# Kernel optimization log

Measured on AMD Instinct MI355X. Metric: run time of the kernel, lower is better.

Reference implementation:

```python
import jax, jax.numpy as jnp
import numpy as np

N, CIN, COUT, H, W, K = 2, 64, 64, 256, 512, 3


def _gen_sphere_position(height, width, Kh, Kw):
    # Faithful numpy port of SphereConv.gen_sphere_position (ERP type).
    delta_lat = np.pi / height
    delta_lon = 2 * np.pi / width
    range_x = np.arange(-(Kw // 2), Kw // 2 + 1)
    if not Kw % 2:
        range_x = np.delete(range_x, Kw // 2)
    range_y = np.arange(-(Kh // 2), Kh // 2 + 1)
    if not Kh % 2:
        range_y = np.delete(range_y, Kh // 2)
    kerX = np.tan(range_x * delta_lon)
    kerY = np.tan(range_y * delta_lat) / np.cos(range_y * delta_lon)
    kerX, kerY = np.meshgrid(kerX, kerY)
    rho = np.sqrt(kerX ** 2 + kerY ** 2)
    if Kh % 2 and Kw % 2:
        rho[Kh // 2][Kw // 2] = 1e-08
    nu = np.arctan(rho)
    cos_nu, sin_nu = np.cos(nu), np.sin(nu)
    lat_range = (np.arange(height) / height - 0.5) * np.pi
    lon_range = (np.arange(width) / width - 0.5) * (2 * np.pi)
    lat = np.array([np.arcsin(cos_nu * np.sin(l) + kerY * sin_nu * np.cos(l) / rho) for l in lat_range])  # (H,Kh,Kw)
    lat = np.array([lat for _ in lon_range]).transpose((1, 0, 2, 3))  # (H,W,Kh,Kw)
    lon = np.array([np.arctan2(kerX * sin_nu, rho * np.cos(l) * cos_nu - kerY * np.sin(l) * sin_nu) for l in lat_range])  # (H,Kh,Kw)
    lon = np.array([lon + _lon for _lon in lon_range]).transpose((1, 0, 2, 3))  # (H,W,Kh,Kw)
    lat = (lat / np.pi + 0.5) * height
    lon = (lon / (2 * np.pi) + 0.5) * width % width
    LatLon = np.stack((lat, lon)).astype(np.float32)  # (2,H,W,Kh,Kw)
    LatLon = LatLon.transpose((3, 4, 0, 1, 2)).reshape(Kh * Kw * 2, height, width)  # channel = (i*Kw+j)*2 + {0:lat,1:lon}
    return LatLon


def setup_inputs() -> dict:
    key = jax.random.key(0)
    kx, kw = jax.random.split(key)
    x = jax.random.normal(kx, (N, CIN, H, W), dtype=jnp.float32)
    n = CIN * K * K
    stdv = 1.0 / np.sqrt(n)
    weight = jax.random.uniform(kw, (COUT, CIN, K, K), dtype=jnp.float32, minval=-stdv, maxval=stdv)
    position = jnp.asarray(_gen_sphere_position(H, W, K, K))  # (2*K*K, H, W)
    return {"x": x, "weight": weight, "position": position}


def _sphere_conv(x, weight, position):
    # x: [N,C,H,W]; position: [2*K2,Hout,Wout] absolute (lat=y, lon=x) sample coords per kernel tap.
    Cout, Cin, Kh, Kw = weight.shape
    K2 = Kh * Kw
    Hi, Wi = x.shape[2], x.shape[3]
    pos = position.reshape(K2, 2, position.shape[-2], position.shape[-1])
    py, px = pos[:, 0], pos[:, 1]  # [K2,Hout,Wout]
    y0 = jnp.floor(py)
    x0 = jnp.floor(px)
    dy = py - y0
    dx = px - x0

    def corner(yi, xi, wgt):
        valid = (yi >= 0) & (yi <= Hi - 1) & (xi >= 0) & (xi <= Wi - 1)
        yc = jnp.clip(yi, 0, Hi - 1).astype(jnp.int32)
        xc = jnp.clip(xi, 0, Wi - 1).astype(jnp.int32)
        v = x[:, :, yc, xc]  # gather -> [N,C,K2,Hout,Wout]
        return v * (wgt * valid)[None, None]

    sampled = (corner(y0, x0, (1 - dy) * (1 - dx))
               + corner(y0, x0 + 1, (1 - dy) * dx)
               + corner(y0 + 1, x0, dy * (1 - dx))
               + corner(y0 + 1, x0 + 1, dy * dx))  # [N,C,K2,Hout,Wout]
    w = weight.reshape(Cout, Cin, K2)
    return jnp.einsum('ock,nckhw->nohw', w, sampled)


def reference(x, weight, position):
    return _sphere_conv(x, weight, position)
```

## Files before the change

kernel.cpp:

```cpp
#include <hip/hip_runtime.h>
#include <hip/hip_bf16.h>


constexpr int N_ = 2;
constexpr int CIN = 64;
constexpr int COUT = 64;
constexpr int H_ = 256;
constexpr int W_ = 512;
constexpr int K2 = 9;
constexpr int HW = H_ * W_;
constexpr int NSTEP = (CIN * K2) / 32;
constexpr int PTILE = 128;
constexpr int SROW = 40;

typedef __attribute__((ext_vector_type(8))) short short8;
typedef __attribute__((ext_vector_type(4))) float floatx4;
typedef __attribute__((ext_vector_type(2))) float floatx2;

__device__ __forceinline__ float bfhi2f(unsigned u) {
  return __uint_as_float(u);
}

__global__ void prep_w(const float* __restrict__ w, ushort* __restrict__ wTr) {
  int i = blockIdx.x * blockDim.x + threadIdx.x;
  if (i >= 4 * NSTEP * 64 * 8) return;
  int j = i & 7;
  int lane = (i >> 3) & 63;
  int s = (i >> 9) % NSTEP;
  int wv = i / (512 * NSTEP);
  int o = wv * 16 + (lane & 15);
  int kk = s * 32 + (lane >> 4) * 8 + j;
  int tap = kk >> 6, c = kk & 63;
  __hip_bfloat16 b = __float2bfloat16(w[(o * CIN + c) * K2 + tap]);
  wTr[i] = *(ushort*)&b;
}

__global__ __launch_bounds__(256) void transpose_x(
    const float* __restrict__ x, ushort* __restrict__ xt) {
  __shared__ ushort tile[64 * 72];
  int b = blockIdx.x;
  int n = b >> 11;
  int hw0 = (b & 2047) * 64;
  int tid = threadIdx.x;
  int px = tid & 63, c4 = tid >> 6;
  const float* xn = x + (size_t)n * CIN * HW;
#pragma unroll
  for (int it = 0; it < 16; ++it) {
    int c = it * 4 + c4;
    float v = xn[(size_t)c * HW + hw0 + px];
    __hip_bfloat16 hb = __float2bfloat16(v);
    tile[px * 72 + c] = *(ushort*)&hb;
  }
  __syncthreads();
  ushort* xtn = xt + (size_t)n * HW * CIN;
#pragma unroll
  for (int it = 0; it < 2; ++it) {
    int task = it * 256 + tid;
    int px2 = task >> 3, chunk = task & 7;
    uint4 v = *(uint4*)&tile[px2 * 72 + chunk * 8];
    *(uint4*)&xtn[(size_t)(hw0 + px2) * 64 + chunk * 8] = v;
  }
}

__global__ __launch_bounds__(256, 3) void sphere_conv_mfma(
    const ushort* __restrict__ xt, const ushort* __restrict__ wTr,
    const float* __restrict__ pos, float* __restrict__ out) {
  __shared__ int off_lds[K2 * PTILE];
  __shared__ uint2 wgt_lds[K2 * PTILE];
  __shared__ ushort sbuf[2][PTILE * SROW];

  int tid = threadIdx.x;
  int blk = blockIdx.x;
  int n = blk >> 10;
  int ptile = (blk & 1023) * PTILE;

  for (int i = tid; i < K2 * PTILE; i += 256) {
    int t = i / PTILE, p = i - t * PTILE;
    int hw = ptile + p;
    float py = pos[(2 * t + 0) * HW + hw];
    float px = pos[(2 * t + 1) * HW + hw];
    float y0f = floorf(py), x0f = floorf(px);
    float dy = py - y0f, dx = px - x0f;
    float y1f = y0f + 1.f, x1f = x0f + 1.f;
    float vy0 = (y0f >= 0.f && y0f <= (float)(H_ - 1)) ? 1.f : 0.f;
    float vy1 = (y1f >= 0.f && y1f <= (float)(H_ - 1)) ? 1.f : 0.f;
    float vx0 = (x0f >= 0.f && x0f <= (float)(W_ - 1)) ? 1.f : 0.f;
    float vx1 = (x1f >= 0.f && x1f <= (float)(W_ - 1)) ? 1.f : 0.f;
    float w00 = (1.f - dy) * (1.f - dx) * vy0 * vx0;
    float w01 = (1.f - dy) * dx * vy0 * vx1;
    float w10 = dy * (1.f - dx) * vy1 * vx0;
    float w11 = dy * dx * vy1 * vx1;
    int y0c = (int)fminf(fmaxf(y0f, 0.f), (float)(H_ - 1));
    int y1c = (int)fminf(fmaxf(y1f, 0.f), (float)(H_ - 1));
    int x0c = (int)fminf(fmaxf(x0f, 0.f), (float)(W_ - 1));
    int x1c = (int)fminf(fmaxf(x1f, 0.f), (float)(W_ - 1));
    int o00 = y0c * W_ + x0c;
    off_lds[i] = o00 | ((x1c - x0c) << 20) | ((y1c - y0c) << 21);
    __hip_bfloat16 b00 = __float2bfloat16(w00), b01 = __float2bfloat16(w01);
    __hip_bfloat16 b10 = __float2bfloat16(w10), b11 = __float2bfloat16(w11);
    unsigned lo = ((unsigned)*(ushort*)&b01 << 16) | *(ushort*)&b00;
    unsigned hi = ((unsigned)*(ushort*)&b11 << 16) | *(ushort*)&b10;
    wgt_lds[i] = make_uint2(lo, hi);
  }

  int lane = tid & 63, wv = tid >> 6;
  int col = lane & 15, quad = lane >> 4;
  int px_s = tid >> 1, hf = tid & 1;

  floatx4 acc[8];
#pragma unroll
  for (int nt = 0; nt < 8; ++nt) acc[nt] = (floatx4)0.f;

  const ushort* xtn = xt + (size_t)n * HW * CIN;

  __syncthreads();

  auto gather = [&](int s, short8 g[8], float w4[4]) {
    int t = s >> 1;
    int c0 = ((s & 1) << 5) + (hf << 4);
    int pk = off_lds[t * PTILE + px_s];
    uint2 wr = wgt_lds[t * PTILE + px_s];
    w4[0] = bfhi2f(wr.x << 16);
    w4[1] = bfhi2f(wr.x & 0xFFFF0000u);
    w4[2] = bfhi2f(wr.y << 16);
    w4[3] = bfhi2f(wr.y & 0xFFFF0000u);
    int o00 = pk & 0x1FFFF;
    int dx1 = (pk >> 20) & 1;
    int dyW = ((pk >> 21) & 1) * W_;
    const ushort* base = xtn + c0;
    const ushort* p00 = base + (size_t)o00 * 64;
    const ushort* p01 = p00 + dx1 * 64;
    const ushort* p10 = p00 + dyW * 64;
    const ushort* p11 = p10 + dx1 * 64;
    g[0] = *(const short8*)p00; g[1] = *(const short8*)(p00 + 8);
    g[2] = *(const short8*)p01; g[3] = *(const short8*)(p01 + 8);
    g[4] = *(const short8*)p10; g[5] = *(const short8*)(p10 + 8);
    g[6] = *(const short8*)p11; g[7] = *(const short8*)(p11 + 8);
  };

  short8 gA[8];
  float wA[4];
  gather(0, gA, wA);

#pragma unroll
  for (int s = 0; s < NSTEP; ++s) {
    short8 gB[8];
    float wB[4];
    if (s + 1 < NSTEP) gather(s + 1, gB, wB);

    const unsigned* u = (const unsigned*)gA;
    floatx2 a2[8];
#pragma unroll
    for (int d = 0; d < 8; ++d) {
      floatx2 f = {bfhi2f(u[d] << 16), bfhi2f(u[d] & 0xFFFF0000u)};
      a2[d] = floatx2{wA[0], wA[0]} * f;
    }
#pragma unroll
    for (int c = 1; c < 4; ++c) {
#pragma unroll
      for (int d = 0; d < 8; ++d) {
        unsigned v = u[c * 8 + d];
        floatx2 f = {bfhi2f(v << 16), bfhi2f(v & 0xFFFF0000u)};
        a2[d] = __builtin_elementwise_fma(floatx2{wA[c], wA[c]}, f, a2[d]);
      }
    }
    __align__(16) unsigned tmp[8];
#pragma unroll
    for (int d = 0; d < 8; ++d) {
      __hip_bfloat16 lo = __float2bfloat16(a2[d].x);
      __hip_bfloat16 hi = __float2bfloat16(a2[d].y);
      tmp[d] = ((unsigned)*(ushort*)&hi << 16) | *(ushort*)&lo;
    }
    uint4* dst = (uint4*)&sbuf[s & 1][px_s * SROW + hf * 16];
    dst[0] = ((const uint4*)tmp)[0];
    dst[1] = ((const uint4*)tmp)[1];

    __syncthreads();

    short8 afrag = *(const short8*)(wTr + ((wv * NSTEP + s) * 64 + lane) * 8);
#pragma unroll
    for (int nt = 0; nt < 8; ++nt) {
      short8 bfrag = *(const short8*)&sbuf[s & 1][(nt * 16 + col) * SROW + quad * 8];
      acc[nt] = __builtin_amdgcn_mfma_f32_16x16x32_bf16(afrag, bfrag, acc[nt], 0, 0, 0);
    }

    if (s + 1 < NSTEP) {
#pragma unroll
      for (int q = 0; q < 8; ++q) gA[q] = gB[q];
#pragma unroll
      for (int q = 0; q < 4; ++q) wA[q] = wB[q];
    }
  }

#pragma unroll
  for (int nt = 0; nt < 8; ++nt) {
#pragma unroll
    for (int r = 0; r < 4; ++r) {
      int o = wv * 16 + quad * 4 + r;
      out[(size_t)(n * COUT + o) * HW + ptile + nt * 16 + col] = acc[nt][r];
    }
  }
}

extern "C" void kernel_launch(void* const* d_in, const int* in_sizes, int n_in,
                              void* d_out, int out_size, void* d_ws, size_t ws_size,
                              hipStream_t stream) {
  const float* x   = (const float*)d_in[0];
  const float* w   = (const float*)d_in[1];
  const float* pos = (const float*)d_in[2];
  float* out = (float*)d_out;

  ushort* wTr = (ushort*)d_ws;
  ushort* xt = (ushort*)((char*)d_ws + (128 << 10));

  prep_w<<<(4 * NSTEP * 64 * 8 + 255) / 256, 256, 0, stream>>>(w, wTr);
  transpose_x<<<N_ * (HW / 64), 256, 0, stream>>>(x, xt);

  int nblk = N_ * (HW / PTILE);
  sphere_conv_mfma<<<nblk, 256, 0, stream>>>(xt, wTr, pos, out);
}
```

Baseline: 208.8 us.

## Gather bilinear samples directly into MFMA B fragments, removing LDS staging

The main kernel now has each wave own 32 output pixels and all 64 output channels. Each lane gathers and interpolates its own 8-channel slice straight into the MFMA B-fragment layout, so the LDS offset/weight tables, the LDS sample buffer and the per-step block barriers are gone. Positions are decoded per lane in registers, and occupancy is raised to 4 blocks per SIMD. The transpose kernel also switches to float4 loads. In exchange, each lane reloads the weight A-fragments from global memory at every step, the position math is recomputed per lane, and the explicit prefetch of the next step's gathers is lost.

```diff
diff --git a/kernel.cpp b/kernel.cpp
--- a/kernel.cpp
+++ b/kernel.cpp
@@ -11,7 +11,6 @@
 constexpr int HW = H_ * W_;
 constexpr int NSTEP = (CIN * K2) / 32;
 constexpr int PTILE = 128;
-constexpr int SROW = 40;
 
 typedef __attribute__((ext_vector_type(8))) short short8;
 typedef __attribute__((ext_vector_type(4))) float floatx4;
@@ -27,8 +26,8 @@
   int j = i & 7;
   int lane = (i >> 3) & 63;
   int s = (i >> 9) % NSTEP;
-  int wv = i / (512 * NSTEP);
-  int o = wv * 16 + (lane & 15);
+  int ot = i / (512 * NSTEP);
+  int o = ot * 16 + (lane & 15);
   int kk = s * 32 + (lane >> 4) * 8 + j;
   int tap = kk >> 6, c = kk & 63;
   __hip_bfloat16 b = __float2bfloat16(w[(o * CIN + c) * K2 + tap]);
@@ -42,14 +41,21 @@
   int n = b >> 11;
   int hw0 = (b & 2047) * 64;
   int tid = threadIdx.x;
-  int px = tid & 63, c4 = tid >> 6;
+  int px4 = (tid & 15) * 4;
+  int cq = tid >> 4;
   const float* xn = x + (size_t)n * CIN * HW;
 #pragma unroll
-  for (int it = 0; it < 16; ++it) {
-    int c = it * 4 + c4;
-    float v = xn[(size_t)c * HW + hw0 + px];
-    __hip_bfloat16 hb = __float2bfloat16(v);
-    tile[px * 72 + c] = *(ushort*)&hb;
+  for (int it = 0; it < 4; ++it) {
+    int c = it * 16 + cq;
+    float4 v = *(const float4*)&xn[(size_t)c * HW + hw0 + px4];
+    __hip_bfloat16 b0 = __float2bfloat16(v.x);
+    __hip_bfloat16 b1 = __float2bfloat16(v.y);
+    __hip_bfloat16 b2 = __float2bfloat16(v.z);
+    __hip_bfloat16 b3 = __float2bfloat16(v.w);
+    tile[(px4 + 0) * 72 + c] = *(ushort*)&b0;
+    tile[(px4 + 1) * 72 + c] = *(ushort*)&b1;
+    tile[(px4 + 2) * 72 + c] = *(ushort*)&b2;
+    tile[(px4 + 3) * 72 + c] = *(ushort*)&b3;
   }
   __syncthreads();
   ushort* xtn = xt + (size_t)n * HW * CIN;
@@ -62,144 +68,123 @@
   }
 }
 
-__global__ __launch_bounds__(256, 3) void sphere_conv_mfma(
+__global__ __launch_bounds__(256, 4) void sphere_conv_mfma(
     const ushort* __restrict__ xt, const ushort* __restrict__ wTr,
     const float* __restrict__ pos, float* __restrict__ out) {
-  __shared__ int off_lds[K2 * PTILE];
-  __shared__ uint2 wgt_lds[K2 * PTILE];
-  __shared__ ushort sbuf[2][PTILE * SROW];
-
   int tid = threadIdx.x;
   int blk = blockIdx.x;
   int n = blk >> 10;
   int ptile = (blk & 1023) * PTILE;
-
-  for (int i = tid; i < K2 * PTILE; i += 256) {
-    int t = i / PTILE, p = i - t * PTILE;
-    int hw = ptile + p;
-    float py = pos[(2 * t + 0) * HW + hw];
-    float px = pos[(2 * t + 1) * HW + hw];
-    float y0f = floorf(py), x0f = floorf(px);
-    float dy = py - y0f, dx = px - x0f;
-    float y1f = y0f + 1.f, x1f = x0f + 1.f;
-    float vy0 = (y0f >= 0.f && y0f <= (float)(H_ - 1)) ? 1.f : 0.f;
-    float vy1 = (y1f >= 0.f && y1f <= (float)(H_ - 1)) ? 1.f : 0.f;
-    float vx0 = (x0f >= 0.f && x0f <= (float)(W_ - 1)) ? 1.f : 0.f;
-    float vx1 = (x1f >= 0.f && x1f <= (float)(W_ - 1)) ? 1.f : 0.f;
-    float w00 = (1.f - dy) * (1.f - dx) * vy0 * vx0;
-    float w01 = (1.f - dy) * dx * vy0 * vx1;
-    float w10 = dy * (1.f - dx) * vy1 * vx0;
-    float w11 = dy * dx * vy1 * vx1;
-    int y0c = (int)fminf(fmaxf(y0f, 0.f), (float)(H_ - 1));
-    int y1c = (int)fminf(fmaxf(y1f, 0.f), (float)(H_ - 1));
-    int x0c = (int)fminf(fmaxf(x0f, 0.f), (float)(W_ - 1));
-    int x1c = (int)fminf(fmaxf(x1f, 0.f), (float)(W_ - 1));
-    int o00 = y0c * W_ + x0c;
-    off_lds[i] = o00 | ((x1c - x0c) << 20) | ((y1c - y0c) << 21);
-    __hip_bfloat16 b00 = __float2bfloat16(w00), b01 = __float2bfloat16(w01);
-    __hip_bfloat16 b10 = __float2bfloat16(w10), b11 = __float2bfloat16(w11);
-    unsigned lo = ((unsigned)*(ushort*)&b01 << 16) | *(ushort*)&b00;
-    unsigned hi = ((unsigned)*(ushort*)&b11 << 16) | *(ushort*)&b10;
-    wgt_lds[i] = make_uint2(lo, hi);
-  }
-
   int lane = tid & 63, wv = tid >> 6;
   int col = lane & 15, quad = lane >> 4;
-  int px_s = tid >> 1, hf = tid & 1;
-
-  floatx4 acc[8];
-#pragma unroll
-  for (int nt = 0; nt < 8; ++nt) acc[nt] = (floatx4)0.f;
+
+  int hw[2];
+  hw[0] = ptile + wv * 32 + col;
+  hw[1] = hw[0] + 16;
 
   const ushort* xtn = xt + (size_t)n * HW * CIN;
 
-  __syncthreads();
-
-  auto gather = [&](int s, short8 g[8], float w4[4]) {
-    int t = s >> 1;
-    int c0 = ((s & 1) << 5) + (hf << 4);
-    int pk = off_lds[t * PTILE + px_s];
-    uint2 wr = wgt_lds[t * PTILE + px_s];
-    w4[0] = bfhi2f(wr.x << 16);
-    w4[1] = bfhi2f(wr.x & 0xFFFF0000u);
-    w4[2] = bfhi2f(wr.y << 16);
-    w4[3] = bfhi2f(wr.y & 0xFFFF0000u);
-    int o00 = pk & 0x1FFFF;
-    int dx1 = (pk >> 20) & 1;
-    int dyW = ((pk >> 21) & 1) * W_;
-    const ushort* base = xtn + c0;
-    const ushort* p00 = base + (size_t)o00 * 64;
-    const ushort* p01 = p00 + dx1 * 64;
-    const ushort* p10 = p00 + dyW * 64;
-    const ushort* p11 = p10 + dx1 * 64;
-    g[0] = *(const short8*)p00; g[1] = *(const short8*)(p00 + 8);
-    g[2] = *(const short8*)p01; g[3] = *(const short8*)(p01 + 8);
-    g[4] = *(const short8*)p10; g[5] = *(const short8*)(p10 + 8);
-    g[6] = *(const short8*)p11; g[7] = *(const short8*)(p11 + 8);
-  };
-
-  short8 gA[8];
-  float wA[4];
-  gather(0, gA, wA);
+  floatx4 acc[2][4];
+#pragma unroll
+  for (int T = 0; T < 2; ++T)
+#pragma unroll
+    for (int ot = 0; ot < 4; ++ot) acc[T][ot] = (floatx4)0.f;
+
+  int o00[2], dxo[2], dyo[2];
+  float w4[2][4];
 
 #pragma unroll
   for (int s = 0; s < NSTEP; ++s) {
-    short8 gB[8];
-    float wB[4];
-    if (s + 1 < NSTEP) gather(s + 1, gB, wB);
-
-    const unsigned* u = (const unsigned*)gA;
-    floatx2 a2[8];
-#pragma unroll
-    for (int d = 0; d < 8; ++d) {
-      floatx2 f = {bfhi2f(u[d] << 16), bfhi2f(u[d] & 0xFFFF0000u)};
-      a2[d] = floatx2{wA[0], wA[0]} * f;
+    if ((s & 1) == 0) {
+      int t = s >> 1;
+#pragma unroll
+      for (int T = 0; T < 2; ++T) {
+        float py = pos[(2 * t + 0) * HW + hw[T]];
+        float pxx = pos[(2 * t + 1) * HW + hw[T]];
+        float y0f = floorf(py), x0f = floorf(pxx);
+        float dy = py - y0f, dx = pxx - x0f;
+        float y1f = y0f + 1.f, x1f = x0f + 1.f;
+        float vy0 = (y0f >= 0.f && y0f <= (float)(H_ - 1)) ? 1.f : 0.f;
+        float vy1 = (y1f >= 0.f && y1f <= (float)(H_ - 1)) ? 1.f : 0.f;
+        float vx0 = (x0f >= 0.f && x0f <= (float)(W_ - 1)) ? 1.f : 0.f;
+        float vx1 = (x1f >= 0.f && x1f <= (float)(W_ - 1)) ? 1.f : 0.f;
+        w4[T][0] = (1.f - dy) * (1.f - dx) * vy0 * vx0;
+        w4[T][1] = (1.f - dy) * dx * vy0 * vx1;
+        w4[T][2] = dy * (1.f - dx) * vy1 * vx0;
+        w4[T][3] = dy * dx * vy1 * vx1;
+        int y0c = (int)fminf(fmaxf(y0f, 0.f), (float)(H_ - 1));
+        int y1c = (int)fminf(fmaxf(y1f, 0.f), (float)(H_ - 1));
+        int x0c = (int)fminf(fmaxf(x0f, 0.f), (float)(W_ - 1));
+        int x1c = (int)fminf(fmaxf(x1f, 0.f), (float)(W_ - 1));
+        o00[T] = (y0c * W_ + x0c) * CIN;
+        dxo[T] = (x1c - x0c) * CIN;
+        dyo[T] = (y1c - y0c) * (W_ * CIN);
+      }
     }
-#pragma unroll
-    for (int c = 1; c < 4; ++c) {
-#pragma unroll
-      for (int d = 0; d < 8; ++d) {
-        unsigned v = u[c * 8 + d];
-        floatx2 f = {bfhi2f(v << 16), bfhi2f(v & 0xFFFF0000u)};
-        a2[d] = __builtin_elementwise_fma(floatx2{wA[c], wA[c]}, f, a2[d]);
-      }
+    int c0 = ((s & 1) << 5) + (quad << 3);
+
+    short8 g[2][4];
+#pragma unroll
+    for (int T = 0; T < 2; ++T) {
+      const ushort* p00 = xtn + (size_t)o00[T] + c0;
+      const ushort* p10 = p00 + dyo[T];
+      g[T][0] = *(const short8*)p00;
+      g[T][1] = *(const short8*)(p00 + dxo[T]);
+      g[T][2] = *(const short8*)p10;
+      g[T][3] = *(const short8*)(p10 + dxo[T]);
     }
-    __align__(16) unsigned tmp[8];
-#pragma unroll
-    for (int d = 0; d < 8; ++d) {
-      __hip_bfloat16 lo = __float2bfloat16(a2[d].x);
-      __hip_bfloat16 hi = __float2bfloat16(a2[d].y);
-      tmp[d] = ((unsigned)*(ushort*)&hi << 16) | *(ushort*)&lo;
+
+    short8 afr[4];
+#pragma unroll
+    for (int ot = 0; ot < 4; ++ot)
+      afr[ot] = *(const short8*)(wTr + ((size_t)(ot * NSTEP + s) * 64 + lane) * 8);
+
+    short8 bfr[2];
+#pragma unroll
+    for (int T = 0; T < 2; ++T) {
+      const unsigned* u = (const unsigned*)&g[T][0];
+      floatx2 a2[4];
+#pragma unroll
+      for (int d = 0; d < 4; ++d) {
+        floatx2 f = {bfhi2f(u[d] << 16), bfhi2f(u[d] & 0xFFFF0000u)};
+        a2[d] = floatx2{w4[T][0], w4[T][0]} * f;
+      }
+#pragma unroll
+      for (int c = 1; c < 4; ++c) {
+#pragma unroll
+        for (int d = 0; d < 4; ++d) {
+          unsigned v = u[c * 4 + d];
+          floatx2 f = {bfhi2f(v << 16), bfhi2f(v & 0xFFFF0000u)};
+          a2[d] = __builtin_elementwise_fma(floatx2{w4[T][c], w4[T][c]}, f, a2[d]);
+        }
+      }
+      union { unsigned q[4]; short8 s8; } pk;
+#pragma unroll
+      for (int d = 0; d < 4; ++d) {
+        __hip_bfloat16 lo = __float2bfloat16(a2[d].x);
+        __hip_bfloat16 hi = __float2bfloat16(a2[d].y);
+        pk.q[d] = ((unsigned)*(ushort*)&hi << 16) | *(ushort*)&lo;
+      }
+      bfr[T] = pk.s8;
     }
-    uint4* dst = (uint4*)&sbuf[s & 1][px_s * SROW + hf * 16];
-    dst[0] = ((const uint4*)tmp)[0];
-    dst[1] = ((const uint4*)tmp)[1];
-
-    __syncthreads();
-
-    short8 afrag = *(const short8*)(wTr + ((wv * NSTEP + s) * 64 + lane) * 8);
-#pragma unroll
-    for (int nt = 0; nt < 8; ++nt) {
-      short8 bfrag = *(const short8*)&sbuf[s & 1][(nt * 16 + col) * SROW + quad * 8];
-      acc[nt] = __builtin_amdgcn_mfma_f32_16x16x32_bf16(afrag, bfrag, acc[nt], 0, 0, 0);
-    }
-
-    if (s + 1 < NSTEP) {
-#pragma unroll
-      for (int q = 0; q < 8; ++q) gA[q] = gB[q];
-#pragma unroll
-      for (int q = 0; q < 4; ++q) wA[q] = wB[q];
-    }
+
+#pragma unroll
+    for (int T = 0; T < 2; ++T)
+#pragma unroll
+      for (int ot = 0; ot < 4; ++ot)
+        acc[T][ot] = __builtin_amdgcn_mfma_f32_16x16x32_bf16(afr[ot], bfr[T], acc[T][ot], 0, 0, 0);
   }
 
 #pragma unroll
-  for (int nt = 0; nt < 8; ++nt) {
-#pragma unroll
-    for (int r = 0; r < 4; ++r) {
-      int o = wv * 16 + quad * 4 + r;
-      out[(size_t)(n * COUT + o) * HW + ptile + nt * 16 + col] = acc[nt][r];
-    }
-  }
+  for (int T = 0; T < 2; ++T)
+#pragma unroll
+    for (int ot = 0; ot < 4; ++ot)
+#pragma unroll
+      for (int r = 0; r < 4; ++r) {
+        int o = ot * 16 + quad * 4 + r;
+        out[(size_t)(n * COUT + o) * HW + ptile + wv * 32 + T * 16 + col] =
+            acc[T][ot][r];
+      }
 }
 
 extern "C" void kernel_launch(void* const* d_in, const int* in_sizes, int n_in,
```

Result: slower. 304.2 us (+45.7%).
